# Optimization experiments

Hardware: AMD Instinct MI355X
Metric: run time of the kernel (lower is better)

Reference implementation:

```python
import jax, jax.numpy as jnp
import numpy as np

NUM_HEADS = 12
STEP_SIZE = 3

def softmax_1(a):
    # exp(a_i) / (1 + sum_j exp(a_j)), numerically stable
    m = jnp.maximum(jnp.max(a, axis=-1, keepdims=True), 0.0)
    e = jnp.exp(a - m)
    return e / (jnp.exp(-m) + jnp.sum(e, axis=-1, keepdims=True))

def setup_inputs() -> dict:
    key = jax.random.key(0)
    ks = jax.random.split(key, 7)
    B, N, C, L = 16, 4096, 768, 16
    s = C ** -0.5
    return {
        "x": jax.random.normal(ks[0], (B, N, C), dtype=jnp.float32),
        "query": jax.random.normal(ks[1], (1, L, C), dtype=jnp.float32),
        "Wq": jax.random.normal(ks[2], (C, C), dtype=jnp.float32) * s,
        "Wk": jax.random.normal(ks[3], (C, C), dtype=jnp.float32) * s,
        "Wv": jax.random.normal(ks[4], (C, C), dtype=jnp.float32) * s,
        "Wproj": jax.random.normal(ks[5], (C, C), dtype=jnp.float32) * s,
        "b_proj": jnp.zeros((C,), dtype=jnp.float32),
    }

def reference(x, query, Wq, Wk, Wv, Wproj, b_proj):
    B, N, C = x.shape
    H = NUM_HEADS
    hd = C // H
    L = query.shape[1]
    scale = hd ** -0.5
    # learned queries broadcast over batch
    queries = jnp.broadcast_to(query, (B, L, C))
    q = (queries @ Wq.T).reshape(B, L, H, hd).transpose(0, 2, 1, 3)  # [B,H,L,hd]
    k = (x @ Wk.T).reshape(B, N, H, hd).transpose(0, 2, 1, 3)        # [B,H,N,hd]
    v = k  # Hopfield update: state retrieves against stored patterns k
    for _ in range(STEP_SIZE):
        qs = q * scale
        attn = jnp.einsum('bhld,bhnd->bhln', qs, k)  # [B,H,L,N]
        attn = softmax_1(attn)
        q = jnp.einsum('bhln,bhnd->bhld', attn, v)   # [B,H,L,hd]
    out = q.transpose(0, 2, 1, 3).reshape(B, L, C)
    out = out @ Wv.T          # self.v output projection (no bias)
    out = out @ Wproj.T + b_proj  # self.proj
    return out
```

## Files before the change

### kernel.cpp

```cpp
#include <hip/hip_runtime.h>


typedef float  float4v  __attribute__((ext_vector_type(4)));
typedef short  short4v  __attribute__((ext_vector_type(4)));
typedef short  short8v  __attribute__((ext_vector_type(8)));
typedef unsigned int uint4v __attribute__((ext_vector_type(4)));
typedef short8v bf16x8;

#define NC 8

__device__ __forceinline__ unsigned short f2bf_hi(float f){
  unsigned int u = __float_as_uint(f);
  u += 0x7fffu + ((u >> 16) & 1u);
  return (unsigned short)(u >> 16);
}
__device__ __forceinline__ float bf2f(unsigned short h){
  return __uint_as_float(((unsigned int)h) << 16);
}

__global__ __launch_bounds__(256)
void cvt_w_kernel(const float* __restrict__ w, unsigned short* __restrict__ wh,
                  unsigned short* __restrict__ wl){
  int idx = blockIdx.x*256 + threadIdx.x;
  float4v v = ((const float4v*)w)[idx];
  short4v h4, l4;
  #pragma unroll
  for(int e=0;e<4;e++){
    unsigned short hh = f2bf_hi(v[e]);
    h4[e] = (short)hh;
    l4[e] = (short)f2bf_hi(v[e] - bf2f(hh));
  }
  ((short4v*)wh)[idx] = h4;
  ((short4v*)wl)[idx] = l4;
}

__global__ __launch_bounds__(256)
void q0_kernel(const float* __restrict__ query, const float* __restrict__ wq,
               float* __restrict__ q0){
  int idx = blockIdx.x*256 + threadIdx.x;
  int l = idx / 768, c = idx - l*768;
  const float* qr = query + l*768;
  const float* wr = wq + (size_t)c*768;
  float s = 0.f;
  for(int j=0;j<768;j+=4){
    float4v a  = *(const float4v*)(qr+j);
    float4v w4 = *(const float4v*)(wr+j);
    s += a[0]*w4[0]+a[1]*w4[1]+a[2]*w4[2]+a[3]*w4[3];
  }
  q0[idx] = s;
}

__global__ __launch_bounds__(256, 2)
void gemm_k_kernel(const float* __restrict__ x, const unsigned short* __restrict__ wh,
                   const unsigned short* __restrict__ wl, float* __restrict__ kout){
  __shared__ unsigned short Ah[128*40], Al[128*40];
  __shared__ unsigned short Bh[128*48], Bl[128*48];
  const int tid  = threadIdx.x;
  const int bm   = blockIdx.x;
  const int bn   = blockIdx.y;
  const int wave = tid >> 6, lane = tid & 63, quad = lane >> 4, l16 = lane & 15;
  const int wm   = (wave >> 1)*64, wn = (wave & 1)*64;

  float4v acc[4][4];
  #pragma unroll
  for(int i=0;i<4;i++)
    #pragma unroll
    for(int j=0;j<4;j++) acc[i][j] = (float4v){0.f,0.f,0.f,0.f};

  const float* xA = x + (size_t)bm*128*768;
  const unsigned short* wBh = wh + (size_t)bn*128*768;
  const unsigned short* wBl = wl + (size_t)bn*128*768;

  for(int k0=0;k0<768;k0+=32){
    __syncthreads();
    #pragma unroll
    for(int i=0;i<4;i++){
      int fi = tid + i*256;
      int row = fi >> 3, c4 = fi & 7;
      float4v va = *(const float4v*)(xA + (size_t)row*768 + k0 + c4*4);
      short4v ha, la;
      #pragma unroll
      for(int e=0;e<4;e++){
        unsigned short hh = f2bf_hi(va[e]);
        ha[e] = (short)hh;
        la[e] = (short)f2bf_hi(va[e] - bf2f(hh));
      }
      *(short4v*)(Ah + row*40 + c4*4) = ha;
      *(short4v*)(Al + row*40 + c4*4) = la;
    }
    #pragma unroll
    for(int i=0;i<2;i++){
      int ci = tid + i*256;
      int row = ci >> 2, c16 = ci & 3;
      *(short8v*)(Bh + row*48 + c16*8) = *(const short8v*)(wBh + (size_t)row*768 + k0 + c16*8);
      *(short8v*)(Bl + row*48 + c16*8) = *(const short8v*)(wBl + (size_t)row*768 + k0 + c16*8);
    }
    __syncthreads();

    bf16x8 a_h[4], a_l[4], b_h[4], b_l[4];
    #pragma unroll
    for(int i=0;i<4;i++){
      int ar = wm + i*16 + l16;
      a_h[i] = *(const bf16x8*)(Ah + ar*40 + quad*8);
      a_l[i] = *(const bf16x8*)(Al + ar*40 + quad*8);
      int br = wn + i*16 + l16;
      b_h[i] = *(const bf16x8*)(Bh + br*48 + quad*8);
      b_l[i] = *(const bf16x8*)(Bl + br*48 + quad*8);
    }
    #pragma unroll
    for(int i=0;i<4;i++)
      #pragma unroll
      for(int j=0;j<4;j++){
        acc[i][j] = __builtin_amdgcn_mfma_f32_16x16x32_bf16(a_h[i], b_h[j], acc[i][j],0,0,0);
        acc[i][j] = __builtin_amdgcn_mfma_f32_16x16x32_bf16(a_l[i], b_h[j], acc[i][j],0,0,0);
        acc[i][j] = __builtin_amdgcn_mfma_f32_16x16x32_bf16(a_h[i], b_l[j], acc[i][j],0,0,0);
      }
  }
  const size_t cbase = (size_t)(bm*128)*768 + (size_t)bn*128;
  #pragma unroll
  for(int i=0;i<4;i++)
    #pragma unroll
    for(int j=0;j<4;j++)
      #pragma unroll
      for(int r=0;r<4;r++)
        kout[cbase + (size_t)(wm + i*16 + quad*4 + r)*768 + wn + j*16 + l16] = acc[i][j][r];
}

__global__ __launch_bounds__(256, 4)
void attn_step_kernel(const float* __restrict__ kbuf, const float* __restrict__ qsrc,
                      long qb_stride, float* __restrict__ qacc, float* __restrict__ lacc){
  __shared__ unsigned int knd[64*68];
  __shared__ unsigned int kdn[64*65];
  __shared__ float p_s[16*68];
  __shared__ float red[4][16];

  const int tid  = threadIdx.x;
  const int c    = blockIdx.x;
  const int h    = blockIdx.y;
  const int b    = blockIdx.z;
  const int wave = tid >> 6, lane = tid & 63, quad = lane >> 4, l16 = lane & 15;

  const float* kb = kbuf + ((size_t)b*4096 + (size_t)c*(4096/NC))*768 + h*64;

  const float* qp = qsrc + (size_t)b*qb_stride + (size_t)l16*768 + h*64;
  bf16x8 qh[2], ql[2];
  #pragma unroll
  for(int s = 0; s < 2; ++s){
    float4v v0 = *(const float4v*)(qp + s*32 + quad*8);
    float4v v1 = *(const float4v*)(qp + s*32 + quad*8 + 4);
    #pragma unroll
    for(int e = 0; e < 8; ++e){
      float v = (e < 4 ? v0[e] : v1[e-4]) * 0.125f;
      unsigned short hh = f2bf_hi(v);
      qh[s][e] = (short)hh;
      ql[s][e] = (short)f2bf_hi(v - bf2f(hh));
    }
  }

  float4v acc = (float4v){0.f,0.f,0.f,0.f};
  float lsum = 0.f;

  const int sn = tid >> 2;
  const int dq = tid & 3;

  for(int t = 0; t < (4096/NC)/64; ++t){
    const float* src = kb + (size_t)(t*64 + sn)*768 + dq*16;
    #pragma unroll
    for(int g = 0; g < 4; ++g){
      float4v va = *(const float4v*)(src + g*4);
      unsigned int pk0, pk1, pk2, pk3;
      {
        unsigned short hh0 = f2bf_hi(va[0]); pk0 = (unsigned)hh0 | ((unsigned)f2bf_hi(va[0]-bf2f(hh0)) << 16);
        unsigned short hh1 = f2bf_hi(va[1]); pk1 = (unsigned)hh1 | ((unsigned)f2bf_hi(va[1]-bf2f(hh1)) << 16);
        unsigned short hh2 = f2bf_hi(va[2]); pk2 = (unsigned)hh2 | ((unsigned)f2bf_hi(va[2]-bf2f(hh2)) << 16);
        unsigned short hh3 = f2bf_hi(va[3]); pk3 = (unsigned)hh3 | ((unsigned)f2bf_hi(va[3]-bf2f(hh3)) << 16);
      }
      *(uint4v*)(knd + sn*68 + dq*16 + g*4) = (uint4v){pk0, pk1, pk2, pk3};
      const int dbase = dq*16 + g*4;
      kdn[(dbase+0)*65 + sn] = pk0;
      kdn[(dbase+1)*65 + sn] = pk1;
      kdn[(dbase+2)*65 + sn] = pk2;
      kdn[(dbase+3)*65 + sn] = pk3;
    }
    __syncthreads();

    float4v sfr = (float4v){0.f,0.f,0.f,0.f};
    #pragma unroll
    for(int s = 0; s < 2; ++s){
      const unsigned int* ap = knd + (wave*16 + l16)*68 + s*32 + quad*8;
      uint4v w0 = *(const uint4v*)ap;
      uint4v w1 = *(const uint4v*)(ap + 4);
      bf16x8 a_h, a_l;
      #pragma unroll
      for(int j = 0; j < 4; ++j){
        a_h[j]   = (short)(w0[j] & 0xffffu);  a_l[j]   = (short)(w0[j] >> 16);
        a_h[j+4] = (short)(w1[j] & 0xffffu);  a_l[j+4] = (short)(w1[j] >> 16);
      }
      sfr = __builtin_amdgcn_mfma_f32_16x16x32_bf16(a_h, qh[s], sfr, 0,0,0);
      sfr = __builtin_amdgcn_mfma_f32_16x16x32_bf16(a_l, qh[s], sfr, 0,0,0);
      sfr = __builtin_amdgcn_mfma_f32_16x16x32_bf16(a_h, ql[s], sfr, 0,0,0);
    }
    float4v p;
    #pragma unroll
    for(int r = 0; r < 4; ++r) p[r] = __expf(sfr[r]);
    lsum += p[0] + p[1] + p[2] + p[3];
    *(float4v*)(p_s + l16*68 + wave*16 + quad*4) = p;
    __syncthreads();

    #pragma unroll
    for(int s = 0; s < 2; ++s){
      const float* pp = p_s + l16*68 + s*32 + quad*8;
      float4v p0 = *(const float4v*)pp;
      float4v p1 = *(const float4v*)(pp + 4);
      bf16x8 pa_h, pa_l;
      #pragma unroll
      for(int e = 0; e < 8; ++e){
        float v = (e < 4 ? p0[e] : p1[e-4]);
        unsigned short hh = f2bf_hi(v);
        pa_h[e] = (short)hh;
        pa_l[e] = (short)f2bf_hi(v - bf2f(hh));
      }
      const unsigned int* bp = kdn + (wave*16 + l16)*65 + s*32 + quad*8;
      bf16x8 kb_h, kb_l;
      #pragma unroll
      for(int j = 0; j < 8; ++j){
        unsigned int w = bp[j];
        kb_h[j] = (short)(w & 0xffffu);
        kb_l[j] = (short)(w >> 16);
      }
      acc = __builtin_amdgcn_mfma_f32_16x16x32_bf16(pa_h, kb_h, acc, 0,0,0);
      acc = __builtin_amdgcn_mfma_f32_16x16x32_bf16(pa_l, kb_h, acc, 0,0,0);
      acc = __builtin_amdgcn_mfma_f32_16x16x32_bf16(pa_h, kb_l, acc, 0,0,0);
    }
    __syncthreads();
  }

  lsum += __shfl_xor(lsum, 16);
  lsum += __shfl_xor(lsum, 32);
  if(quad == 0) red[wave][l16] = lsum;
  __syncthreads();
  if(tid < 16){
    float tot = red[0][tid] + red[1][tid] + red[2][tid] + red[3][tid];
    atomicAdd(&lacc[(b*12 + h)*16 + tid], tot);
  }
  #pragma unroll
  for(int r = 0; r < 4; ++r){
    atomicAdd(&qacc[(size_t)(b*16 + quad*4 + r)*768 + h*64 + wave*16 + l16], acc[r]);
  }
}

__global__ __launch_bounds__(256)
void attn_norm_kernel(float* __restrict__ qacc, float* __restrict__ lacc,
                      float* __restrict__ qcur){
  __shared__ float lt[16];
  const int bh = blockIdx.x, b = bh/12, h = bh - (bh/12)*12, tid = threadIdx.x;
  if(tid < 16) lt[tid] = 1.f + lacc[bh*16 + tid];
  __syncthreads();
  if(tid < 16) lacc[bh*16 + tid] = 0.f;
  for(int idx = tid; idx < 1024; idx += 256){
    int l = idx >> 6, d = idx & 63;
    size_t a = (size_t)(b*16 + l)*768 + h*64 + d;
    qcur[a] = qacc[a] / lt[l];
    qacc[a] = 0.f;
  }
}

__global__ __launch_bounds__(256)
void proj_kernel(const float* __restrict__ inp, const float* __restrict__ w,
                 const float* __restrict__ bias, float* __restrict__ out){
  __shared__ float rows[4*768];
  const int r0 = blockIdx.x*4;
  const int c  = blockIdx.y*256 + threadIdx.x;
  for(int j = threadIdx.x; j < 4*768; j += 256) rows[j] = inp[(size_t)r0*768 + j];
  __syncthreads();
  const float* wr = w + (size_t)c*768;
  float a0=0.f, a1=0.f, a2=0.f, a3=0.f;
  for(int j=0;j<768;j+=4){
    float4v w4 = *(const float4v*)(wr+j);
    float4v r0v = *(const float4v*)(rows+j);
    float4v r1v = *(const float4v*)(rows+768+j);
    float4v r2v = *(const float4v*)(rows+1536+j);
    float4v r3v = *(const float4v*)(rows+2304+j);
    #pragma unroll
    for(int e=0;e<4;e++){
      a0 += r0v[e]*w4[e]; a1 += r1v[e]*w4[e];
      a2 += r2v[e]*w4[e]; a3 += r3v[e]*w4[e];
    }
  }
  const float bb = bias ? bias[c] : 0.f;
  out[(size_t)(r0+0)*768 + c] = a0 + bb;
  out[(size_t)(r0+1)*768 + c] = a1 + bb;
  out[(size_t)(r0+2)*768 + c] = a2 + bb;
  out[(size_t)(r0+3)*768 + c] = a3 + bb;
}

extern "C" void kernel_launch(void* const* d_in, const int* in_sizes, int n_in,
                              void* d_out, int out_size, void* d_ws, size_t ws_size,
                              hipStream_t stream){
  const float* x     = (const float*)d_in[0];
  const float* query = (const float*)d_in[1];
  const float* Wq    = (const float*)d_in[2];
  const float* Wk    = (const float*)d_in[3];
  const float* Wv    = (const float*)d_in[4];
  const float* Wproj = (const float*)d_in[5];
  const float* bproj = (const float*)d_in[6];
  float* out = (float*)d_out;

  char* ws = (char*)d_ws;
  float*          kbuf = (float*)(ws);
  float*          qcur = (float*)(ws + 201326592);
  float*          q0   = (float*)(ws + 202113024);
  char*           R    = ws + 202162176;
  unsigned short* wkh  = (unsigned short*)(R);
  unsigned short* wkl  = (unsigned short*)(R + 1179648);
  float*          qacc = (float*)(R);
  float*          lacc = (float*)(R + 786432);
  float*          out1 = (float*)(R);

  cvt_w_kernel<<<576, 256, 0, stream>>>(Wk, wkh, wkl);
  q0_kernel<<<48, 256, 0, stream>>>(query, Wq, q0);
  gemm_k_kernel<<<dim3(512, 6), 256, 0, stream>>>(x, wkh, wkl, kbuf);

  hipMemsetAsync(qacc, 0, 786432 + 12288, stream);
  dim3 sg(NC, 12, 16);
  attn_step_kernel<<<sg, 256, 0, stream>>>(kbuf, q0,   0,       qacc, lacc);
  attn_norm_kernel<<<192, 256, 0, stream>>>(qacc, lacc, qcur);
  attn_step_kernel<<<sg, 256, 0, stream>>>(kbuf, qcur, 16*768,  qacc, lacc);
  attn_norm_kernel<<<192, 256, 0, stream>>>(qacc, lacc, qcur);
  attn_step_kernel<<<sg, 256, 0, stream>>>(kbuf, qcur, 16*768,  qacc, lacc);
  attn_norm_kernel<<<192, 256, 0, stream>>>(qacc, lacc, qcur);

  proj_kernel<<<dim3(64, 3), 256, 0, stream>>>(qcur, Wv, nullptr, out1);
  proj_kernel<<<dim3(64, 3), 256, 0, stream>>>(out1, Wproj, bproj, out);
}
```

Measured before the change: 760.6 us.

## Store K as packed hi/lo bf16 and optionally pre-split x before GEMM

The K-projection GEMM now writes K as packed hi/lo bf16 pairs, one uint32 each, so the three attention steps read K directly without redoing the float-to-bf16 split every pass. When the workspace is large enough, x is also converted once into planar hi/lo bf16 arrays before the GEMM. The GEMM grid is reordered so that N-blocks vary fastest, which may improve reuse of x across blocks. Pre-splitting x adds a full extra pass over x, writing and then re-reading 200MB, which may cost more than the in-GEMM conversion it replaces.

```diff
diff --git a/kernel.cpp b/kernel.cpp
--- a/kernel.cpp
+++ b/kernel.cpp
@@ -17,12 +17,16 @@
 __device__ __forceinline__ float bf2f(unsigned short h){
   return __uint_as_float(((unsigned int)h) << 16);
 }
+__device__ __forceinline__ unsigned int packbf(float v){
+  unsigned short hh = f2bf_hi(v);
+  return (unsigned)hh | ((unsigned)f2bf_hi(v - bf2f(hh)) << 16);
+}
 
 __global__ __launch_bounds__(256)
-void cvt_w_kernel(const float* __restrict__ w, unsigned short* __restrict__ wh,
-                  unsigned short* __restrict__ wl){
-  int idx = blockIdx.x*256 + threadIdx.x;
-  float4v v = ((const float4v*)w)[idx];
+void cvt_planar_kernel(const float* __restrict__ src, unsigned short* __restrict__ dh,
+                       unsigned short* __restrict__ dl){
+  size_t idx = (size_t)blockIdx.x*256 + threadIdx.x;
+  float4v v = ((const float4v*)src)[idx];
   short4v h4, l4;
   #pragma unroll
   for(int e=0;e<4;e++){
@@ -30,8 +34,8 @@
     h4[e] = (short)hh;
     l4[e] = (short)f2bf_hi(v[e] - bf2f(hh));
   }
-  ((short4v*)wh)[idx] = h4;
-  ((short4v*)wl)[idx] = l4;
+  ((short4v*)dh)[idx] = h4;
+  ((short4v*)dl)[idx] = l4;
 }
 
 __global__ __launch_bounds__(256)
@@ -51,13 +55,14 @@
 }
 
 __global__ __launch_bounds__(256, 2)
-void gemm_k_kernel(const float* __restrict__ x, const unsigned short* __restrict__ wh,
-                   const unsigned short* __restrict__ wl, float* __restrict__ kout){
+void gemm_k_pre_kernel(const unsigned short* __restrict__ xh, const unsigned short* __restrict__ xl,
+                       const unsigned short* __restrict__ wh, const unsigned short* __restrict__ wl,
+                       unsigned int* __restrict__ kout){
   __shared__ unsigned short Ah[128*40], Al[128*40];
   __shared__ unsigned short Bh[128*48], Bl[128*48];
   const int tid  = threadIdx.x;
-  const int bm   = blockIdx.x;
-  const int bn   = blockIdx.y;
+  const int bn   = blockIdx.x;
+  const int bm   = blockIdx.y;
   const int wave = tid >> 6, lane = tid & 63, quad = lane >> 4, l16 = lane & 15;
   const int wm   = (wave >> 1)*64, wn = (wave & 1)*64;
 
@@ -67,33 +72,28 @@
     #pragma unroll
     for(int j=0;j<4;j++) acc[i][j] = (float4v){0.f,0.f,0.f,0.f};
 
-  const float* xA = x + (size_t)bm*128*768;
+  const unsigned short* xAh = xh + (size_t)bm*128*768;
+  const unsigned short* xAl = xl + (size_t)bm*128*768;
   const unsigned short* wBh = wh + (size_t)bn*128*768;
   const unsigned short* wBl = wl + (size_t)bn*128*768;
 
   for(int k0=0;k0<768;k0+=32){
     __syncthreads();
     #pragma unroll
-    for(int i=0;i<4;i++){
+    for(int i=0;i<2;i++){
       int fi = tid + i*256;
-      int row = fi >> 3, c4 = fi & 7;
-      float4v va = *(const float4v*)(xA + (size_t)row*768 + k0 + c4*4);
-      short4v ha, la;
-      #pragma unroll
-      for(int e=0;e<4;e++){
-        unsigned short hh = f2bf_hi(va[e]);
-        ha[e] = (short)hh;
-        la[e] = (short)f2bf_hi(va[e] - bf2f(hh));
-      }
-      *(short4v*)(Ah + row*40 + c4*4) = ha;
-      *(short4v*)(Al + row*40 + c4*4) = la;
+      int row = fi >> 2, c8 = fi & 3;
+      size_t go = (size_t)row*768 + k0 + c8*8;
+      *(short8v*)(Ah + row*40 + c8*8) = *(const short8v*)(xAh + go);
+      *(short8v*)(Al + row*40 + c8*8) = *(const short8v*)(xAl + go);
     }
     #pragma unroll
     for(int i=0;i<2;i++){
       int ci = tid + i*256;
-      int row = ci >> 2, c16 = ci & 3;
-      *(short8v*)(Bh + row*48 + c16*8) = *(const short8v*)(wBh + (size_t)row*768 + k0 + c16*8);
-      *(short8v*)(Bl + row*48 + c16*8) = *(const short8v*)(wBl + (size_t)row*768 + k0 + c16*8);
+      int row = ci >> 2, c8 = ci & 3;
+      size_t go = (size_t)row*768 + k0 + c8*8;
+      *(short8v*)(Bh + row*48 + c8*8) = *(const short8v*)(wBh + go);
+      *(short8v*)(Bl + row*48 + c8*8) = *(const short8v*)(wBl + go);
     }
     __syncthreads();
 
@@ -123,11 +123,88 @@
     for(int j=0;j<4;j++)
       #pragma unroll
       for(int r=0;r<4;r++)
-        kout[cbase + (size_t)(wm + i*16 + quad*4 + r)*768 + wn + j*16 + l16] = acc[i][j][r];
+        kout[cbase + (size_t)(wm + i*16 + quad*4 + r)*768 + wn + j*16 + l16] = packbf(acc[i][j][r]);
+}
+
+__global__ __launch_bounds__(256, 2)
+void gemm_k_fly_kernel(const float* __restrict__ x, const unsigned short* __restrict__ wh,
+                       const unsigned short* __restrict__ wl, unsigned int* __restrict__ kout){
+  __shared__ unsigned short Ah[128*40], Al[128*40];
+  __shared__ unsigned short Bh[128*48], Bl[128*48];
+  const int tid  = threadIdx.x;
+  const int bn   = blockIdx.x;
+  const int bm   = blockIdx.y;
+  const int wave = tid >> 6, lane = tid & 63, quad = lane >> 4, l16 = lane & 15;
+  const int wm   = (wave >> 1)*64, wn = (wave & 1)*64;
+
+  float4v acc[4][4];
+  #pragma unroll
+  for(int i=0;i<4;i++)
+    #pragma unroll
+    for(int j=0;j<4;j++) acc[i][j] = (float4v){0.f,0.f,0.f,0.f};
+
+  const float* xA = x + (size_t)bm*128*768;
+  const unsigned short* wBh = wh + (size_t)bn*128*768;
+  const unsigned short* wBl = wl + (size_t)bn*128*768;
+
+  for(int k0=0;k0<768;k0+=32){
+    __syncthreads();
+    #pragma unroll
+    for(int i=0;i<4;i++){
+      int fi = tid + i*256;
+      int row = fi >> 3, c4 = fi & 7;
+      float4v va = *(const float4v*)(xA + (size_t)row*768 + k0 + c4*4);
+      short4v ha, la;
+      #pragma unroll
+      for(int e=0;e<4;e++){
+        unsigned short hh = f2bf_hi(va[e]);
+        ha[e] = (short)hh;
+        la[e] = (short)f2bf_hi(va[e] - bf2f(hh));
+      }
+      *(short4v*)(Ah + row*40 + c4*4) = ha;
+      *(short4v*)(Al + row*40 + c4*4) = la;
+    }
+    #pragma unroll
+    for(int i=0;i<2;i++){
+      int ci = tid + i*256;
+      int row = ci >> 2, c8 = ci & 3;
+      size_t go = (size_t)row*768 + k0 + c8*8;
+      *(short8v*)(Bh + row*48 + c8*8) = *(const short8v*)(wBh + go);
+      *(short8v*)(Bl + row*48 + c8*8) = *(const short8v*)(wBl + go);
+    }
+    __syncthreads();
+
+    bf16x8 a_h[4], a_l[4], b_h[4], b_l[4];
+    #pragma unroll
+    for(int i=0;i<4;i++){
+      int ar = wm + i*16 + l16;
+      a_h[i] = *(const bf16x8*)(Ah + ar*40 + quad*8);
+      a_l[i] = *(const bf16x8*)(Al + ar*40 + quad*8);
+      int br = wn + i*16 + l16;
+      b_h[i] = *(const bf16x8*)(Bh + br*48 + quad*8);
+      b_l[i] = *(const bf16x8*)(Bl + br*48 + quad*8);
+    }
+    #pragma unroll
+    for(int i=0;i<4;i++)
+      #pragma unroll
+      for(int j=0;j<4;j++){
+        acc[i][j] = __builtin_amdgcn_mfma_f32_16x16x32_bf16(a_h[i], b_h[j], acc[i][j],0,0,0);
+        acc[i][j] = __builtin_amdgcn_mfma_f32_16x16x32_bf16(a_l[i], b_h[j], acc[i][j],0,0,0);
+        acc[i][j] = __builtin_amdgcn_mfma_f32_16x16x32_bf16(a_h[i], b_l[j], acc[i][j],0,0,0);
+      }
+  }
+  const size_t cbase = (size_t)(bm*128)*768 + (size_t)bn*128;
+  #pragma unroll
+  for(int i=0;i<4;i++)
+    #pragma unroll
+    for(int j=0;j<4;j++)
+      #pragma unroll
+      for(int r=0;r<4;r++)
+        kout[cbase + (size_t)(wm + i*16 + quad*4 + r)*768 + wn + j*16 + l16] = packbf(acc[i][j][r]);
 }
 
 __global__ __launch_bounds__(256, 4)
-void attn_step_kernel(const float* __restrict__ kbuf, const float* __restrict__ qsrc,
+void attn_step_kernel(const unsigned int* __restrict__ kbuf, const float* __restrict__ qsrc,
                       long qb_stride, float* __restrict__ qacc, float* __restrict__ lacc){
   __shared__ unsigned int knd[64*68];
   __shared__ unsigned int kdn[64*65];
@@ -140,7 +217,7 @@
   const int b    = blockIdx.z;
   const int wave = tid >> 6, lane = tid & 63, quad = lane >> 4, l16 = lane & 15;
 
-  const float* kb = kbuf + ((size_t)b*4096 + (size_t)c*(4096/NC))*768 + h*64;
+  const unsigned int* kb = kbuf + ((size_t)b*4096 + (size_t)c*(4096/NC))*768 + h*64;
 
   const float* qp = qsrc + (size_t)b*qb_stride + (size_t)l16*768 + h*64;
   bf16x8 qh[2], ql[2];
@@ -164,23 +241,16 @@
   const int dq = tid & 3;
 
   for(int t = 0; t < (4096/NC)/64; ++t){
-    const float* src = kb + (size_t)(t*64 + sn)*768 + dq*16;
+    const unsigned int* src = kb + (size_t)(t*64 + sn)*768 + dq*16;
     #pragma unroll
     for(int g = 0; g < 4; ++g){
-      float4v va = *(const float4v*)(src + g*4);
-      unsigned int pk0, pk1, pk2, pk3;
-      {
-        unsigned short hh0 = f2bf_hi(va[0]); pk0 = (unsigned)hh0 | ((unsigned)f2bf_hi(va[0]-bf2f(hh0)) << 16);
-        unsigned short hh1 = f2bf_hi(va[1]); pk1 = (unsigned)hh1 | ((unsigned)f2bf_hi(va[1]-bf2f(hh1)) << 16);
-        unsigned short hh2 = f2bf_hi(va[2]); pk2 = (unsigned)hh2 | ((unsigned)f2bf_hi(va[2]-bf2f(hh2)) << 16);
-        unsigned short hh3 = f2bf_hi(va[3]); pk3 = (unsigned)hh3 | ((unsigned)f2bf_hi(va[3]-bf2f(hh3)) << 16);
-      }
-      *(uint4v*)(knd + sn*68 + dq*16 + g*4) = (uint4v){pk0, pk1, pk2, pk3};
+      uint4v pk = *(const uint4v*)(src + g*4);
+      *(uint4v*)(knd + sn*68 + dq*16 + g*4) = pk;
       const int dbase = dq*16 + g*4;
-      kdn[(dbase+0)*65 + sn] = pk0;
-      kdn[(dbase+1)*65 + sn] = pk1;
-      kdn[(dbase+2)*65 + sn] = pk2;
-      kdn[(dbase+3)*65 + sn] = pk3;
+      kdn[(dbase+0)*65 + sn] = pk[0];
+      kdn[(dbase+1)*65 + sn] = pk[1];
+      kdn[(dbase+2)*65 + sn] = pk[2];
+      kdn[(dbase+3)*65 + sn] = pk[3];
     }
     __syncthreads();
 
@@ -306,30 +376,65 @@
   const float* bproj = (const float*)d_in[6];
   float* out = (float*)d_out;
 
+  const size_t XB   = 100663296;
+  const size_t KB_  = 201326592;
+  const size_t PRE_NEED = 2*XB + KB_ + 786432 + 49152 + 2359296;
+
   char* ws = (char*)d_ws;
-  float*          kbuf = (float*)(ws);
-  float*          qcur = (float*)(ws + 201326592);
-  float*          q0   = (float*)(ws + 202113024);
-  char*           R    = ws + 202162176;
-  unsigned short* wkh  = (unsigned short*)(R);
-  unsigned short* wkl  = (unsigned short*)(R + 1179648);
-  float*          qacc = (float*)(R);
-  float*          lacc = (float*)(R + 786432);
-  float*          out1 = (float*)(R);
-
-  cvt_w_kernel<<<576, 256, 0, stream>>>(Wk, wkh, wkl);
-  q0_kernel<<<48, 256, 0, stream>>>(query, Wq, q0);
-  gemm_k_kernel<<<dim3(512, 6), 256, 0, stream>>>(x, wkh, wkl, kbuf);
-
-  hipMemsetAsync(qacc, 0, 786432 + 12288, stream);
-  dim3 sg(NC, 12, 16);
-  attn_step_kernel<<<sg, 256, 0, stream>>>(kbuf, q0,   0,       qacc, lacc);
-  attn_norm_kernel<<<192, 256, 0, stream>>>(qacc, lacc, qcur);
-  attn_step_kernel<<<sg, 256, 0, stream>>>(kbuf, qcur, 16*768,  qacc, lacc);
-  attn_norm_kernel<<<192, 256, 0, stream>>>(qacc, lacc, qcur);
-  attn_step_kernel<<<sg, 256, 0, stream>>>(kbuf, qcur, 16*768,  qacc, lacc);
-  attn_norm_kernel<<<192, 256, 0, stream>>>(qacc, lacc, qcur);
-
-  proj_kernel<<<dim3(64, 3), 256, 0, stream>>>(qcur, Wv, nullptr, out1);
-  proj_kernel<<<dim3(64, 3), 256, 0, stream>>>(out1, Wproj, bproj, out);
-}
+  if(ws_size >= PRE_NEED){
+    unsigned short* xh   = (unsigned short*)(ws);
+    unsigned short* xl   = (unsigned short*)(ws + XB);
+    unsigned int*   kbuf = (unsigned int*)  (ws + 2*XB);
+    float*          qcur = (float*)(ws + 2*XB + KB_);
+    float*          q0   = (float*)(ws + 2*XB + KB_ + 786432);
+    char*           R    = ws + 2*XB + KB_ + 786432 + 49152;
+    unsigned short* wkh  = (unsigned short*)(R);
+    unsigned short* wkl  = (unsigned short*)(R + 1179648);
+    float*          qacc = (float*)(R);
+    float*          lacc = (float*)(R + 786432);
+    float*          out1 = (float*)(R);
+
+    cvt_planar_kernel<<<576, 256, 0, stream>>>(Wk, wkh, wkl);
+    cvt_planar_kernel<<<49152, 256, 0, stream>>>(x, xh, xl);
+    q0_kernel<<<48, 256, 0, stream>>>(query, Wq, q0);
+    gemm_k_pre_kernel<<<dim3(6, 512), 256, 0, stream>>>(xh, xl, wkh, wkl, kbuf);
+
+    hipMemsetAsync(qacc, 0, 786432 + 12288, stream);
+    dim3 sg(NC, 12, 16);
+    attn_step_kernel<<<sg, 256, 0, stream>>>(kbuf, q0,   0,       qacc, lacc);
+    attn_norm_kernel<<<192, 256, 0, stream>>>(qacc, lacc, qcur);
+    attn_step_kernel<<<sg, 256, 0, stream>>>(kbuf, qcur, 16*768,  qacc, lacc);
+    attn_norm_kernel<<<192, 256, 0, stream>>>(qacc, lacc, qcur);
+    attn_step_kernel<<<sg, 256, 0, stream>>>(kbuf, qcur, 16*768,  qacc, lacc);
+    attn_norm_kernel<<<192, 256, 0, stream>>>(qacc, lacc, qcur);
+
+    proj_kernel<<<dim3(64, 3), 256, 0, stream>>>(qcur, Wv, nullptr, out1);
+    proj_kernel<<<dim3(64, 3), 256, 0, stream>>>(out1, Wproj, bproj, out);
+  } else {
+    unsigned int*   kbuf = (unsigned int*)(ws);
+    float*          qcur = (float*)(ws + 201326592);
+    float*          q0   = (float*)(ws + 202113024);
+    char*           R    = ws + 202162176;
+    unsigned short* wkh  = (unsigned short*)(R);
+    unsigned short* wkl  = (unsigned short*)(R + 1179648);
+    float*          qacc = (float*)(R);
+    float*          lacc = (float*)(R + 786432);
+    float*          out1 = (float*)(R);
+
+    cvt_planar_kernel<<<576, 256, 0, stream>>>(Wk, wkh, wkl);
+    q0_kernel<<<48, 256, 0, stream>>>(query, Wq, q0);
+    gemm_k_fly_kernel<<<dim3(6, 512), 256, 0, stream>>>(x, wkh, wkl, kbuf);
+
+    hipMemsetAsync(qacc, 0, 786432 + 12288, stream);
+    dim3 sg(NC, 12, 16);
+    attn_step_kernel<<<sg, 256, 0, stream>>>(kbuf, q0,   0,       qacc, lacc);
+    attn_norm_kernel<<<192, 256, 0, stream>>>(qacc, lacc, qcur);
+    attn_step_kernel<<<sg, 256, 0, stream>>>(kbuf, qcur, 16*768,  qacc, lacc);
+    attn_norm_kernel<<<192, 256, 0, stream>>>(qacc, lacc, qcur);
+    attn_step_kernel<<<sg, 256, 0, stream>>>(kbuf, qcur, 16*768,  qacc, lacc);
+    attn_norm_kernel<<<192, 256, 0, stream>>>(qacc, lacc, qcur);
+
+    proj_kernel<<<dim3(64, 3), 256, 0, stream>>>(qcur, Wv, nullptr, out1);
+    proj_kernel<<<dim3(64, 3), 256, 0, stream>>>(out1, Wproj, bproj, out);
+  }
+}
```

Result: slower. 841.0 us (+10.6%).

## Store K as packed bf16 hi/lo pairs and restructure GEMM tiling

Applied to the files above, without the earlier changes.

The K-projection GEMM now writes K as packed bf16 hi/lo words, so the three attention steps no longer re-split fp32 K and no longer build a transposed LDS copy. The second matmul instead reads columns from the single row-major LDS tile. The GEMM drops its shared-memory B tile: each wave loads its 32 weight columns straight into registers, and blocks are ordered so neighbouring row tiles land on the same XCD. NC doubles to 16 and occupancy hints are raised. The strided column reads from LDS may cause bank conflicts, and the GEMM now reads weights from global memory per wave.

```diff
diff --git a/kernel.cpp b/kernel.cpp
--- a/kernel.cpp
+++ b/kernel.cpp
@@ -7,7 +7,7 @@
 typedef unsigned int uint4v __attribute__((ext_vector_type(4)));
 typedef short8v bf16x8;
 
-#define NC 8
+#define NC 16
 
 __device__ __forceinline__ unsigned short f2bf_hi(float f){
   unsigned int u = __float_as_uint(f);
@@ -17,12 +17,16 @@
 __device__ __forceinline__ float bf2f(unsigned short h){
   return __uint_as_float(((unsigned int)h) << 16);
 }
+__device__ __forceinline__ unsigned int packbf(float v){
+  unsigned short hh = f2bf_hi(v);
+  return (unsigned)hh | ((unsigned)f2bf_hi(v - bf2f(hh)) << 16);
+}
 
 __global__ __launch_bounds__(256)
-void cvt_w_kernel(const float* __restrict__ w, unsigned short* __restrict__ wh,
-                  unsigned short* __restrict__ wl){
-  int idx = blockIdx.x*256 + threadIdx.x;
-  float4v v = ((const float4v*)w)[idx];
+void cvt_planar_kernel(const float* __restrict__ src, unsigned short* __restrict__ dh,
+                       unsigned short* __restrict__ dl){
+  size_t idx = (size_t)blockIdx.x*256 + threadIdx.x;
+  float4v v = ((const float4v*)src)[idx];
   short4v h4, l4;
   #pragma unroll
   for(int e=0;e<4;e++){
@@ -30,8 +34,8 @@
     h4[e] = (short)hh;
     l4[e] = (short)f2bf_hi(v[e] - bf2f(hh));
   }
-  ((short4v*)wh)[idx] = h4;
-  ((short4v*)wl)[idx] = l4;
+  ((short4v*)dh)[idx] = h4;
+  ((short4v*)dl)[idx] = l4;
 }
 
 __global__ __launch_bounds__(256)
@@ -50,87 +54,83 @@
   q0[idx] = s;
 }
 
-__global__ __launch_bounds__(256, 2)
+__global__ __launch_bounds__(256, 3)
 void gemm_k_kernel(const float* __restrict__ x, const unsigned short* __restrict__ wh,
-                   const unsigned short* __restrict__ wl, float* __restrict__ kout){
+                   const unsigned short* __restrict__ wl, unsigned int* __restrict__ kout){
   __shared__ unsigned short Ah[128*40], Al[128*40];
-  __shared__ unsigned short Bh[128*48], Bl[128*48];
   const int tid  = threadIdx.x;
-  const int bm   = blockIdx.x;
-  const int bn   = blockIdx.y;
+  const int id   = blockIdx.x;
+  const int xcd  = id & 7, slot = id >> 3;
+  const int bml  = slot / 6;
+  const int bn   = slot - bml*6;
+  const int bm   = xcd*64 + bml;
   const int wave = tid >> 6, lane = tid & 63, quad = lane >> 4, l16 = lane & 15;
-  const int wm   = (wave >> 1)*64, wn = (wave & 1)*64;
-
-  float4v acc[4][4];
-  #pragma unroll
-  for(int i=0;i<4;i++)
-    #pragma unroll
-    for(int j=0;j<4;j++) acc[i][j] = (float4v){0.f,0.f,0.f,0.f};
+
+  float4v acc[8][2];
+  #pragma unroll
+  for(int i=0;i<8;i++)
+    #pragma unroll
+    for(int j=0;j<2;j++) acc[i][j] = (float4v){0.f,0.f,0.f,0.f};
 
   const float* xA = x + (size_t)bm*128*768;
-  const unsigned short* wBh = wh + (size_t)bn*128*768;
-  const unsigned short* wBl = wl + (size_t)bn*128*768;
+  const unsigned short* wbh = wh + (size_t)(bn*128 + wave*32 + l16)*768 + quad*8;
+  const unsigned short* wbl = wl + (size_t)(bn*128 + wave*32 + l16)*768 + quad*8;
 
   for(int k0=0;k0<768;k0+=32){
-    __syncthreads();
-    #pragma unroll
-    for(int i=0;i<4;i++){
+    bf16x8 b_h[2], b_l[2];
+    #pragma unroll
+    for(int j=0;j<2;j++){
+      b_h[j] = *(const bf16x8*)(wbh + (size_t)j*16*768 + k0);
+      b_l[j] = *(const bf16x8*)(wbl + (size_t)j*16*768 + k0);
+    }
+    __syncthreads();
+    #pragma unroll
+    for(int i=0;i<2;i++){
       int fi = tid + i*256;
-      int row = fi >> 3, c4 = fi & 7;
-      float4v va = *(const float4v*)(xA + (size_t)row*768 + k0 + c4*4);
-      short4v ha, la;
+      int row = fi >> 2, c8 = fi & 3;
+      const float* sp = xA + (size_t)row*768 + k0 + c8*8;
+      float4v va = *(const float4v*)sp;
+      float4v vb = *(const float4v*)(sp + 4);
+      short8v hv, lv;
       #pragma unroll
       for(int e=0;e<4;e++){
         unsigned short hh = f2bf_hi(va[e]);
-        ha[e] = (short)hh;
-        la[e] = (short)f2bf_hi(va[e] - bf2f(hh));
-      }
-      *(short4v*)(Ah + row*40 + c4*4) = ha;
-      *(short4v*)(Al + row*40 + c4*4) = la;
-    }
-    #pragma unroll
-    for(int i=0;i<2;i++){
-      int ci = tid + i*256;
-      int row = ci >> 2, c16 = ci & 3;
-      *(short8v*)(Bh + row*48 + c16*8) = *(const short8v*)(wBh + (size_t)row*768 + k0 + c16*8);
-      *(short8v*)(Bl + row*48 + c16*8) = *(const short8v*)(wBl + (size_t)row*768 + k0 + c16*8);
-    }
-    __syncthreads();
-
-    bf16x8 a_h[4], a_l[4], b_h[4], b_l[4];
-    #pragma unroll
-    for(int i=0;i<4;i++){
-      int ar = wm + i*16 + l16;
-      a_h[i] = *(const bf16x8*)(Ah + ar*40 + quad*8);
-      a_l[i] = *(const bf16x8*)(Al + ar*40 + quad*8);
-      int br = wn + i*16 + l16;
-      b_h[i] = *(const bf16x8*)(Bh + br*48 + quad*8);
-      b_l[i] = *(const bf16x8*)(Bl + br*48 + quad*8);
-    }
-    #pragma unroll
-    for(int i=0;i<4;i++)
-      #pragma unroll
-      for(int j=0;j<4;j++){
-        acc[i][j] = __builtin_amdgcn_mfma_f32_16x16x32_bf16(a_h[i], b_h[j], acc[i][j],0,0,0);
-        acc[i][j] = __builtin_amdgcn_mfma_f32_16x16x32_bf16(a_l[i], b_h[j], acc[i][j],0,0,0);
-        acc[i][j] = __builtin_amdgcn_mfma_f32_16x16x32_bf16(a_h[i], b_l[j], acc[i][j],0,0,0);
-      }
-  }
-  const size_t cbase = (size_t)(bm*128)*768 + (size_t)bn*128;
-  #pragma unroll
-  for(int i=0;i<4;i++)
-    #pragma unroll
-    for(int j=0;j<4;j++)
+        hv[e] = (short)hh; lv[e] = (short)f2bf_hi(va[e] - bf2f(hh));
+        unsigned short hh2 = f2bf_hi(vb[e]);
+        hv[e+4] = (short)hh2; lv[e+4] = (short)f2bf_hi(vb[e] - bf2f(hh2));
+      }
+      *(short8v*)(Ah + row*40 + c8*8) = hv;
+      *(short8v*)(Al + row*40 + c8*8) = lv;
+    }
+    __syncthreads();
+
+    #pragma unroll
+    for(int i=0;i<8;i++){
+      const int ar = i*16 + l16;
+      bf16x8 a_h = *(const bf16x8*)(Ah + ar*40 + quad*8);
+      bf16x8 a_l = *(const bf16x8*)(Al + ar*40 + quad*8);
+      #pragma unroll
+      for(int j=0;j<2;j++){
+        acc[i][j] = __builtin_amdgcn_mfma_f32_16x16x32_bf16(a_h, b_h[j], acc[i][j],0,0,0);
+        acc[i][j] = __builtin_amdgcn_mfma_f32_16x16x32_bf16(a_l, b_h[j], acc[i][j],0,0,0);
+        acc[i][j] = __builtin_amdgcn_mfma_f32_16x16x32_bf16(a_h, b_l[j], acc[i][j],0,0,0);
+      }
+    }
+  }
+  const size_t cbase = (size_t)(bm*128)*768 + bn*128 + wave*32;
+  #pragma unroll
+  for(int i=0;i<8;i++)
+    #pragma unroll
+    for(int j=0;j<2;j++)
       #pragma unroll
       for(int r=0;r<4;r++)
-        kout[cbase + (size_t)(wm + i*16 + quad*4 + r)*768 + wn + j*16 + l16] = acc[i][j][r];
-}
-
-__global__ __launch_bounds__(256, 4)
-void attn_step_kernel(const float* __restrict__ kbuf, const float* __restrict__ qsrc,
+        kout[cbase + (size_t)(i*16 + quad*4 + r)*768 + j*16 + l16] = packbf(acc[i][j][r]);
+}
+
+__global__ __launch_bounds__(256, 6)
+void attn_step_kernel(const unsigned int* __restrict__ kbuf, const float* __restrict__ qsrc,
                       long qb_stride, float* __restrict__ qacc, float* __restrict__ lacc){
   __shared__ unsigned int knd[64*68];
-  __shared__ unsigned int kdn[64*65];
   __shared__ float p_s[16*68];
   __shared__ float red[4][16];
 
@@ -140,7 +140,7 @@
   const int b    = blockIdx.z;
   const int wave = tid >> 6, lane = tid & 63, quad = lane >> 4, l16 = lane & 15;
 
-  const float* kb = kbuf + ((size_t)b*4096 + (size_t)c*(4096/NC))*768 + h*64;
+  const unsigned int* kb = kbuf + ((size_t)b*4096 + (size_t)c*(4096/NC))*768 + h*64;
 
   const float* qp = qsrc + (size_t)b*qb_stride + (size_t)l16*768 + h*64;
   bf16x8 qh[2], ql[2];
@@ -164,23 +164,10 @@
   const int dq = tid & 3;
 
   for(int t = 0; t < (4096/NC)/64; ++t){
-    const float* src = kb + (size_t)(t*64 + sn)*768 + dq*16;
+    const unsigned int* src = kb + (size_t)(t*64 + sn)*768 + dq*16;
     #pragma unroll
     for(int g = 0; g < 4; ++g){
-      float4v va = *(const float4v*)(src + g*4);
-      unsigned int pk0, pk1, pk2, pk3;
-      {
-        unsigned short hh0 = f2bf_hi(va[0]); pk0 = (unsigned)hh0 | ((unsigned)f2bf_hi(va[0]-bf2f(hh0)) << 16);
-        unsigned short hh1 = f2bf_hi(va[1]); pk1 = (unsigned)hh1 | ((unsigned)f2bf_hi(va[1]-bf2f(hh1)) << 16);
-        unsigned short hh2 = f2bf_hi(va[2]); pk2 = (unsigned)hh2 | ((unsigned)f2bf_hi(va[2]-bf2f(hh2)) << 16);
-        unsigned short hh3 = f2bf_hi(va[3]); pk3 = (unsigned)hh3 | ((unsigned)f2bf_hi(va[3]-bf2f(hh3)) << 16);
-      }
-      *(uint4v*)(knd + sn*68 + dq*16 + g*4) = (uint4v){pk0, pk1, pk2, pk3};
-      const int dbase = dq*16 + g*4;
-      kdn[(dbase+0)*65 + sn] = pk0;
-      kdn[(dbase+1)*65 + sn] = pk1;
-      kdn[(dbase+2)*65 + sn] = pk2;
-      kdn[(dbase+3)*65 + sn] = pk3;
+      *(uint4v*)(knd + sn*68 + dq*16 + g*4) = *(const uint4v*)(src + g*4);
     }
     __syncthreads();
 
@@ -220,11 +207,11 @@
         pa_h[e] = (short)hh;
         pa_l[e] = (short)f2bf_hi(v - bf2f(hh));
       }
-      const unsigned int* bp = kdn + (wave*16 + l16)*65 + s*32 + quad*8;
+      const unsigned int* bp = knd + (size_t)(s*32 + quad*8)*68 + wave*16 + l16;
       bf16x8 kb_h, kb_l;
       #pragma unroll
       for(int j = 0; j < 8; ++j){
-        unsigned int w = bp[j];
+        unsigned int w = bp[j*68];
         kb_h[j] = (short)(w & 0xffffu);
         kb_l[j] = (short)(w >> 16);
       }
@@ -307,7 +294,7 @@
   float* out = (float*)d_out;
 
   char* ws = (char*)d_ws;
-  float*          kbuf = (float*)(ws);
+  unsigned int*   kbuf = (unsigned int*)(ws);
   float*          qcur = (float*)(ws + 201326592);
   float*          q0   = (float*)(ws + 202113024);
   char*           R    = ws + 202162176;
@@ -317,9 +304,9 @@
   float*          lacc = (float*)(R + 786432);
   float*          out1 = (float*)(R);
 
-  cvt_w_kernel<<<576, 256, 0, stream>>>(Wk, wkh, wkl);
+  cvt_planar_kernel<<<576, 256, 0, stream>>>(Wk, wkh, wkl);
   q0_kernel<<<48, 256, 0, stream>>>(query, Wq, q0);
-  gemm_k_kernel<<<dim3(512, 6), 256, 0, stream>>>(x, wkh, wkl, kbuf);
+  gemm_k_kernel<<<3072, 256, 0, stream>>>(x, wkh, wkl, kbuf);
 
   hipMemsetAsync(qacc, 0, 786432 + 12288, stream);
   dim3 sg(NC, 12, 16);
```

Result: faster. 742.2 us (-2.4%).
